# Performance work log

Measured on AMD Instinct MI355X. Metric: run time of the kernel, lower is better.

The kernel has to match this reference:

```python
import jax, jax.numpy as jnp
import numpy as np

EMBED_DIM = 768
NUM_HEADS = 12
HEAD_DIM = EMBED_DIM // NUM_HEADS
HIDDEN_DIM = int(EMBED_DIM * 4.0)
LN_EPS = 1e-5


def setup_inputs() -> dict:
    key = jax.random.key(0)
    ks = jax.random.split(key, 8)
    B, N, C = 16, 1024, EMBED_DIM
    s = 0.02
    return {
        "x": jax.random.normal(ks[0], (B, N, C), dtype=jnp.float32),
        "ln1_g": jnp.ones((C,), jnp.float32),
        "ln1_b": jnp.zeros((C,), jnp.float32),
        "qkv_w": jax.random.normal(ks[1], (C, 3 * C), jnp.float32) * s,
        "qkv_b": jnp.zeros((3 * C,), jnp.float32),
        "proj_w": jax.random.normal(ks[2], (C, C), jnp.float32) * s,
        "proj_b": jnp.zeros((C,), jnp.float32),
        "ln2_g": jnp.ones((C,), jnp.float32),
        "ln2_b": jnp.zeros((C,), jnp.float32),
        "fc1_w": jax.random.normal(ks[3], (C, HIDDEN_DIM), jnp.float32) * s,
        "fc1_b": jnp.zeros((HIDDEN_DIM,), jnp.float32),
        "fc2_w": jax.random.normal(ks[4], (HIDDEN_DIM, C), jnp.float32) * s,
        "fc2_b": jnp.zeros((C,), jnp.float32),
    }


def _layernorm(x, g, b):
    mu = jnp.mean(x, axis=-1, keepdims=True)
    var = jnp.mean(jnp.square(x - mu), axis=-1, keepdims=True)
    return (x - mu) * jax.lax.rsqrt(var + LN_EPS) * g + b


def _attention(x, qkv_w, qkv_b, proj_w, proj_b):
    B, N, C = x.shape
    qkv = x @ qkv_w + qkv_b                       # [B,N,3C]
    qkv = qkv.reshape(B, N, 3, NUM_HEADS, HEAD_DIM)
    q, k, v = qkv[:, :, 0], qkv[:, :, 1], qkv[:, :, 2]  # [B,N,H,D]
    scale = HEAD_DIM ** -0.5
    attn = jnp.einsum("bqhd,bkhd->bhqk", q, k) * scale
    attn = jax.nn.softmax(attn, axis=-1)
    out = jnp.einsum("bhqk,bkhd->bqhd", attn, v).reshape(B, N, C)
    return out @ proj_w + proj_b


def reference(x, ln1_g, ln1_b, qkv_w, qkv_b, proj_w, proj_b,
              ln2_g, ln2_b, fc1_w, fc1_b, fc2_w, fc2_b):
    x = x + _attention(_layernorm(x, ln1_g, ln1_b), qkv_w, qkv_b, proj_w, proj_b)
    h = _layernorm(x, ln2_g, ln2_b)
    h = jax.nn.gelu(h @ fc1_w + fc1_b, approximate=False)
    return x + (h @ fc2_w + fc2_b)
```

## Files before the change

### kernel.cpp

```cpp
#include <hip/hip_runtime.h>
#include <math.h>

#define SEQ 1024
#define NH 12
#define CC 768

using short8 = __attribute__((ext_vector_type(8))) short;
using bf16x8 = __attribute__((ext_vector_type(8))) __bf16;
using f32x4  = __attribute__((ext_vector_type(4))) float;

__device__ __forceinline__ unsigned short f2bf(float f){
  unsigned u = __builtin_bit_cast(unsigned, f);
  u += 0x7FFF + ((u >> 16) & 1);
  return (unsigned short)(u >> 16);
}

__device__ __forceinline__ void gload16(const void* g, void* l){
  __builtin_amdgcn_global_load_lds((const __attribute__((address_space(1))) unsigned int*)g,
                                   (__attribute__((address_space(3))) unsigned int*)l, 16, 0, 0);
}
__device__ __forceinline__ bf16x8 lds_frag(const unsigned short* p){
  return __builtin_bit_cast(bf16x8, *(const short8*)p);
}
__device__ __forceinline__ bf16x8 gld_frag(const unsigned short* p){
  return __builtin_bit_cast(bf16x8, *(const short8*)p);
}

__global__ __launch_bounds__(256) void wtrans(const float* __restrict__ W,
                                              unsigned short* __restrict__ Wt,
                                              int K, int N){
  __shared__ float tile[32][33];
  int tx = threadIdx.x & 31, ty = threadIdx.x >> 5;
  int n0 = blockIdx.x * 32, k0 = blockIdx.y * 32;
#pragma unroll
  for (int j = 0; j < 4; j++)
    tile[ty + j*8][tx] = W[(size_t)(k0 + ty + j*8) * N + n0 + tx];
  __syncthreads();
#pragma unroll
  for (int j = 0; j < 4; j++)
    Wt[(size_t)(n0 + ty + j*8) * K + k0 + tx] = f2bf(tile[tx][ty + j*8]);
}

__global__ __launch_bounds__(64) void ln_k(const float* __restrict__ x,
                                           const float* __restrict__ g,
                                           const float* __restrict__ be,
                                           unsigned short* __restrict__ out){
  const int row = blockIdx.x;
  const int lane = threadIdx.x;
  const float* xr = x + (size_t)row * CC;
  float4 v[3];
  float s = 0.f, sq = 0.f;
#pragma unroll
  for (int j = 0; j < 3; j++){
    v[j] = *(const float4*)(xr + lane*4 + j*256);
    s  += v[j].x + v[j].y + v[j].z + v[j].w;
    sq += v[j].x*v[j].x + v[j].y*v[j].y + v[j].z*v[j].z + v[j].w*v[j].w;
  }
#pragma unroll
  for (int d = 1; d < 64; d <<= 1){ s += __shfl_xor(s, d); sq += __shfl_xor(sq, d); }
  float mu = s * (1.0f/CC);
  float var = sq * (1.0f/CC) - mu*mu;
  float rstd = rsqrtf(var + 1e-5f);
  unsigned short* orow = out + (size_t)row * CC;
#pragma unroll
  for (int j = 0; j < 3; j++){
    int cb = lane*4 + j*256;
    float4 gv = *(const float4*)(g + cb);
    float4 bv = *(const float4*)(be + cb);
    ushort4 o;
    o.x = f2bf((v[j].x - mu)*rstd*gv.x + bv.x);
    o.y = f2bf((v[j].y - mu)*rstd*gv.y + bv.y);
    o.z = f2bf((v[j].z - mu)*rstd*gv.z + bv.z);
    o.w = f2bf((v[j].w - mu)*rstd*gv.w + bv.w);
    *(ushort4*)(orow + cb) = o;
  }
}

__global__ __launch_bounds__(256) void vextract(const unsigned short* __restrict__ qkv,
                                                unsigned short* __restrict__ vT){
  __shared__ unsigned short tile[32][33];
  int bh = blockIdx.y;
  int b = bh / NH, h = bh % NH;
  int tt = blockIdx.x & 31, dt = blockIdx.x >> 5;
  int tx = threadIdx.x & 31, ty = threadIdx.x >> 5;
#pragma unroll
  for (int j = 0; j < 4; j++)
    tile[ty + j*8][tx] = qkv[(size_t)(b*SEQ + tt*32 + ty + j*8)*2304 + 1536 + h*64 + dt*32 + tx];
  __syncthreads();
#pragma unroll
  for (int j = 0; j < 4; j++)
    vT[((size_t)bh*64 + dt*32 + ty + j*8)*SEQ + tt*32 + tx] = tile[tx][ty + j*8];
}

template<int MODE>
__global__ __launch_bounds__(512, 2) void gemm256(const unsigned short* __restrict__ A,
                                                  const unsigned short* __restrict__ Bt,
                                                  const float* __restrict__ bias,
                                                  const float* __restrict__ resid,
                                                  void* __restrict__ outp,
                                                  int M, int N, int K){
  __shared__ __align__(16) unsigned short lds[2][4][128*64];
  const int t = threadIdx.x;
  const int lane = t & 63, w = t >> 6;
  const int wr = w >> 2, wc = w & 3;
  const int l15 = lane & 15, lg = lane >> 4;
  const int mtiles = M >> 8;
  const int cpx = gridDim.x >> 3;
  const int bid = blockIdx.x;
  const int swz = (bid & 7) * cpx + (bid >> 3);
  const int bm = swz % mtiles, bn = swz / mtiles;

  const unsigned short* gA0 = A  + (size_t)bm*256*K;
  const unsigned short* gA1 = gA0 + (size_t)128*K;
  const unsigned short* gB0 = Bt + (size_t)bn*256*K;
  const unsigned short* gB1 = gB0 + (size_t)128*K;

  const int csw = (t & 7) ^ ((t >> 3) & 7);
  const size_t off0 = (size_t)(t >> 3)*K + csw*8;
  const size_t off1 = off0 + (size_t)64*K;

  auto stageh = [&](int bi, int rg, const unsigned short* gb, int kt){
    const unsigned short* s = gb + (size_t)kt*64;
    unsigned short* d = &lds[bi][rg][0];
    gload16(s + off0, d + t*8);
    gload16(s + off1, d + 4096 + t*8);
  };

  const int cx0 = (lg ^ (l15 & 7)) * 8;
  const int cx1 = ((4 + lg) ^ (l15 & 7)) * 8;
  const int rB = (wc & 1)*64 + l15;

  f32x4 acc[8][4] = {};
  const int nk = K >> 6;

  stageh(0,0,gA0,0); stageh(0,1,gA1,0); stageh(0,2,gB0,0); stageh(0,3,gB1,0);
  stageh(1,0,gA0,1); stageh(1,1,gA1,1); stageh(1,2,gB0,1);
  asm volatile("s_waitcnt vmcnt(6)" ::: "memory");
  __builtin_amdgcn_sched_barrier(0);
  __builtin_amdgcn_s_barrier();

  bf16x8 afr[8][2], bfl[2][2], bfh[2][2];
  for (int kt = 0; kt < nk; ++kt){
    const int buf = kt & 1;
    const unsigned short* pA = &lds[buf][wr][0];
    const unsigned short* pB = &lds[buf][2 + (wc >> 1)][0];

#pragma unroll
    for (int m = 0; m < 4; m++){
      afr[m][0] = lds_frag(pA + (m*16 + l15)*64 + cx0);
      afr[m][1] = lds_frag(pA + (m*16 + l15)*64 + cx1);
    }
#pragma unroll
    for (int n = 0; n < 2; n++){
      bfl[n][0] = lds_frag(pB + (rB + n*16)*64 + cx0);
      bfl[n][1] = lds_frag(pB + (rB + n*16)*64 + cx1);
    }
#pragma unroll
    for (int m = 4; m < 8; m++){
      afr[m][0] = lds_frag(pA + (m*16 + l15)*64 + cx0);
      afr[m][1] = lds_frag(pA + (m*16 + l15)*64 + cx1);
    }
    if (kt + 1 < nk) stageh((kt+1)&1, 3, gB1, kt+1);
    __builtin_amdgcn_sched_barrier(0);
    __builtin_amdgcn_s_barrier();
    asm volatile("s_waitcnt lgkmcnt(8)" ::: "memory");
    __builtin_amdgcn_sched_barrier(0);
    __builtin_amdgcn_s_setprio(1);
#pragma unroll
    for (int m = 0; m < 4; m++)
#pragma unroll
      for (int n = 0; n < 2; n++){
        acc[m][n] = __builtin_amdgcn_mfma_f32_16x16x32_bf16(afr[m][0], bfl[n][0], acc[m][n], 0,0,0);
        acc[m][n] = __builtin_amdgcn_mfma_f32_16x16x32_bf16(afr[m][1], bfl[n][1], acc[m][n], 0,0,0);
      }
    __builtin_amdgcn_s_setprio(0);
    __builtin_amdgcn_sched_barrier(0);
    __builtin_amdgcn_s_barrier();

#pragma unroll
    for (int n = 0; n < 2; n++){
      bfh[n][0] = lds_frag(pB + (rB + (n+2)*16)*64 + cx0);
      bfh[n][1] = lds_frag(pB + (rB + (n+2)*16)*64 + cx1);
    }
    if (kt + 2 < nk) stageh(buf, 0, gA0, kt+2);
    __builtin_amdgcn_sched_barrier(0);
    __builtin_amdgcn_s_barrier();
    asm volatile("s_waitcnt lgkmcnt(4)" ::: "memory");
    __builtin_amdgcn_sched_barrier(0);
    __builtin_amdgcn_s_setprio(1);
#pragma unroll
    for (int m = 4; m < 8; m++)
#pragma unroll
      for (int n = 0; n < 2; n++){
        acc[m][n] = __builtin_amdgcn_mfma_f32_16x16x32_bf16(afr[m][0], bfl[n][0], acc[m][n], 0,0,0);
        acc[m][n] = __builtin_amdgcn_mfma_f32_16x16x32_bf16(afr[m][1], bfl[n][1], acc[m][n], 0,0,0);
      }
    __builtin_amdgcn_s_setprio(0);
    __builtin_amdgcn_sched_barrier(0);
    __builtin_amdgcn_s_barrier();

    if (kt + 2 < nk) stageh(buf, 1, gA1, kt+2);
    __builtin_amdgcn_sched_barrier(0);
    __builtin_amdgcn_s_barrier();
    asm volatile("s_waitcnt lgkmcnt(0)" ::: "memory");
    __builtin_amdgcn_sched_barrier(0);
    __builtin_amdgcn_s_setprio(1);
#pragma unroll
    for (int m = 4; m < 8; m++)
#pragma unroll
      for (int n = 0; n < 2; n++){
        acc[m][n+2] = __builtin_amdgcn_mfma_f32_16x16x32_bf16(afr[m][0], bfh[n][0], acc[m][n+2], 0,0,0);
        acc[m][n+2] = __builtin_amdgcn_mfma_f32_16x16x32_bf16(afr[m][1], bfh[n][1], acc[m][n+2], 0,0,0);
      }
    __builtin_amdgcn_s_setprio(0);
    __builtin_amdgcn_sched_barrier(0);
    __builtin_amdgcn_s_barrier();

    if (kt + 2 < nk) stageh(buf, 2, gB0, kt+2);
    __builtin_amdgcn_sched_barrier(0);
    __builtin_amdgcn_s_barrier();
    __builtin_amdgcn_s_setprio(1);
#pragma unroll
    for (int m = 0; m < 4; m++)
#pragma unroll
      for (int n = 0; n < 2; n++){
        acc[m][n+2] = __builtin_amdgcn_mfma_f32_16x16x32_bf16(afr[m][0], bfh[n][0], acc[m][n+2], 0,0,0);
        acc[m][n+2] = __builtin_amdgcn_mfma_f32_16x16x32_bf16(afr[m][1], bfh[n][1], acc[m][n+2], 0,0,0);
      }
    __builtin_amdgcn_s_setprio(0);
    if (kt < nk - 1){
      if (kt + 2 < nk) { asm volatile("s_waitcnt vmcnt(6)" ::: "memory"); }
      else             { asm volatile("s_waitcnt vmcnt(0)" ::: "memory"); }
    }
    __builtin_amdgcn_sched_barrier(0);
    __builtin_amdgcn_s_barrier();
  }

  const int row0 = bm*256 + wr*128 + lg*4;
  const int col0 = bn*256 + wc*64 + l15;
#pragma unroll
  for (int n = 0; n < 4; n++){
    int c = col0 + n*16;
    float bv = bias[c];
#pragma unroll
    for (int m = 0; m < 8; m++){
      int r = row0 + m*16;
#pragma unroll
      for (int i = 0; i < 4; i++){
        size_t idx = (size_t)(r + i) * N + c;
        float v = acc[m][n][i] + bv;
        if constexpr (MODE == 0){
          ((unsigned short*)outp)[idx] = f2bf(v);
        } else if constexpr (MODE == 1){
          ((float*)outp)[idx] = resid[idx] + v;
        } else {
          float u = v + 0.044715f*v*v*v;
          float a = fminf(-1.5957691216057308f*u, 80.f);
          float e = __expf(a);
          float gv = 0.5f*v*(1.0f + (1.f - e)/(1.f + e));
          ((unsigned short*)outp)[idx] = f2bf(gv);
        }
      }
    }
  }
}

__global__ __launch_bounds__(256, 2) void attn_k(const unsigned short* __restrict__ qkv,
                                                 const unsigned short* __restrict__ vT,
                                                 unsigned short* __restrict__ aout){
  __shared__ __align__(16) unsigned short Ks[2][64*64];
  __shared__ __align__(16) unsigned short Vs[2][64*64];
  __shared__ __align__(16) unsigned short Ps[4][32*64];
  const int t = threadIdx.x, lane = t & 63, w = t >> 6;
  const int l15 = lane & 15, lg = lane >> 4;
  const int qt = blockIdx.x;
  const int bh = blockIdx.y;
  const int b = bh / NH, h = bh % NH;
  const size_t qrow0 = (size_t)b * SEQ + qt*128 + w*32;

  bf16x8 qf[2][2];
#pragma unroll
  for (int nf = 0; nf < 2; nf++)
#pragma unroll
    for (int ks = 0; ks < 2; ks++)
      qf[nf][ks] = gld_frag(qkv + (qrow0 + nf*16 + l15)*2304 + h*64 + ks*32 + lg*8);

  f32x4 o[2][4] = {};
  float mold[2] = {-3.0e38f, -3.0e38f};
  float lsum[2] = {0.f, 0.f};

  const unsigned short* Kgl = qkv + (size_t)b * SEQ * 2304 + 768 + h*64;
  const unsigned short* Vgl = vT + (size_t)bh * 64 * SEQ;

  auto stageKV = [&](int bufi, int kt){
#pragma unroll
    for (int i = 0; i < 2; i++){
      int idx = i*256 + t; int r = idx >> 3; int s = idx & 7; int ss = s ^ (r & 7);
      gload16(Kgl + (size_t)(kt*64 + r)*2304 + ss*8, &Ks[bufi][idx*8]);
    }
#pragma unroll
    for (int i = 0; i < 2; i++){
      int idx = i*256 + t; int r = idx >> 3; int s = idx & 7; int ss = s ^ (r & 7);
      gload16(Vgl + (size_t)r*SEQ + kt*64 + ss*8, &Vs[bufi][idx*8]);
    }
  };

  stageKV(0, 0);
  __syncthreads();
  int buf = 0;

  for (int kt = 0; kt < 16; ++kt){
    if (kt + 1 < 16) stageKV(buf ^ 1, kt + 1);

    f32x4 st[4][2] = {};
#pragma unroll
    for (int ks = 0; ks < 2; ks++){
      bf16x8 kf[4];
#pragma unroll
      for (int mf = 0; mf < 4; mf++){
        int rr = mf*16 + l15;
        int sc = (ks*4 + lg) ^ (rr & 7);
        kf[mf] = lds_frag(&Ks[buf][rr*64 + sc*8]);
      }
#pragma unroll
      for (int mf = 0; mf < 4; mf++)
#pragma unroll
        for (int nf = 0; nf < 2; nf++)
          st[mf][nf] = __builtin_amdgcn_mfma_f32_16x16x32_bf16(kf[mf], qf[nf][ks], st[mf][nf], 0, 0, 0);
    }

    float fsc[2];
#pragma unroll
    for (int nf = 0; nf < 2; nf++){
      float mx = -3.0e38f;
#pragma unroll
      for (int mf = 0; mf < 4; mf++)
#pragma unroll
        for (int i = 0; i < 4; i++){
          float sv = st[mf][nf][i] * 0.125f;
          st[mf][nf][i] = sv;
          mx = fmaxf(mx, sv);
        }
      mx = fmaxf(mx, __shfl_xor(mx, 16));
      mx = fmaxf(mx, __shfl_xor(mx, 32));
      float nm = fmaxf(mold[nf], mx);
      float f = __expf(mold[nf] - nm);
      mold[nf] = nm;
      float rs = 0.f;
#pragma unroll
      for (int mf = 0; mf < 4; mf++)
#pragma unroll
        for (int i = 0; i < 4; i++){
          float p = __expf(st[mf][nf][i] - nm);
          st[mf][nf][i] = p;
          rs += p;
        }
      rs += __shfl_xor(rs, 16);
      rs += __shfl_xor(rs, 32);
      lsum[nf] = lsum[nf]*f + rs;
      fsc[nf] = f;
    }

#pragma unroll
    for (int nf = 0; nf < 2; nf++)
#pragma unroll
      for (int mf = 0; mf < 4; mf++)
#pragma unroll
        for (int i = 0; i < 4; i++){
          int rP = nf*16 + l15;
          int col = mf*16 + lg*4 + i;
          Ps[w][rP*64 + (col ^ ((rP & 7) << 3))] = f2bf(st[mf][nf][i]);
        }

#pragma unroll
    for (int mm = 0; mm < 2; mm++)
#pragma unroll
      for (int i = 0; i < 4; i++){
        float fo = __shfl(fsc[mm], lg*4 + i);
#pragma unroll
        for (int df = 0; df < 4; df++)
          o[mm][df][i] *= fo;
      }

#pragma unroll
    for (int ks = 0; ks < 2; ks++){
      bf16x8 pf[2], vf[4];
#pragma unroll
      for (int mm = 0; mm < 2; mm++){
        int rP = mm*16 + l15;
        int sc = (ks*4 + lg) ^ (rP & 7);
        pf[mm] = lds_frag(&Ps[w][rP*64 + sc*8]);
      }
#pragma unroll
      for (int df = 0; df < 4; df++){
        int rr = df*16 + l15;
        int sc = (ks*4 + lg) ^ (rr & 7);
        vf[df] = lds_frag(&Vs[buf][rr*64 + sc*8]);
      }
#pragma unroll
      for (int mm = 0; mm < 2; mm++)
#pragma unroll
        for (int df = 0; df < 4; df++)
          o[mm][df] = __builtin_amdgcn_mfma_f32_16x16x32_bf16(pf[mm], vf[df], o[mm][df], 0, 0, 0);
    }
    __syncthreads();
    buf ^= 1;
  }

#pragma unroll
  for (int mm = 0; mm < 2; mm++){
    float li = 1.0f / lsum[mm];
#pragma unroll
    for (int i = 0; i < 4; i++){
      float rl = __shfl(li, lg*4 + i);
      size_t r = qrow0 + mm*16 + lg*4 + i;
#pragma unroll
      for (int df = 0; df < 4; df++)
        aout[r*CC + h*64 + df*16 + l15] = f2bf(o[mm][df][i] * rl);
    }
  }
}

extern "C" void kernel_launch(void* const* d_in, const int* in_sizes, int n_in,
                              void* d_out, int out_size, void* d_ws, size_t ws_size,
                              hipStream_t stream){
  (void)in_sizes; (void)n_in; (void)out_size; (void)ws_size;
  const float* x      = (const float*)d_in[0];
  const float* ln1_g  = (const float*)d_in[1];
  const float* ln1_b  = (const float*)d_in[2];
  const float* qkv_w  = (const float*)d_in[3];
  const float* qkv_b  = (const float*)d_in[4];
  const float* proj_w = (const float*)d_in[5];
  const float* proj_b = (const float*)d_in[6];
  const float* ln2_g  = (const float*)d_in[7];
  const float* ln2_b  = (const float*)d_in[8];
  const float* fc1_w  = (const float*)d_in[9];
  const float* fc1_b  = (const float*)d_in[10];
  const float* fc2_w  = (const float*)d_in[11];
  const float* fc2_b  = (const float*)d_in[12];
  float* out = (float*)d_out;
  char* ws = (char*)d_ws;

  unsigned short* ln_out  = (unsigned short*)(ws);
  unsigned short* qkv_buf = (unsigned short*)(ws + 25165824);
  unsigned short* vTb     = (unsigned short*)(ws + 100663296);
  unsigned short* attn    = (unsigned short*)(ws + 125829120);
  unsigned short* hbuf    = qkv_buf;
  char* wbase = ws + 150994944;
  unsigned short* wq = (unsigned short*)(wbase);
  unsigned short* wp = (unsigned short*)(wbase + 3538944);
  unsigned short* w1 = (unsigned short*)(wbase + 4718592);
  unsigned short* w2 = (unsigned short*)(wbase + 9437184);

  wtrans<<<dim3(72, 24), 256, 0, stream>>>(qkv_w, wq, 768, 2304);
  wtrans<<<dim3(24, 24), 256, 0, stream>>>(proj_w, wp, 768, 768);
  wtrans<<<dim3(96, 24), 256, 0, stream>>>(fc1_w, w1, 768, 3072);
  wtrans<<<dim3(24, 96), 256, 0, stream>>>(fc2_w, w2, 3072, 768);

  ln_k<<<16384, 64, 0, stream>>>(x, ln1_g, ln1_b, ln_out);
  gemm256<0><<<64*9, 512, 0, stream>>>(ln_out, wq, qkv_b, nullptr, qkv_buf, 16384, 2304, 768);
  vextract<<<dim3(64, 192), 256, 0, stream>>>(qkv_buf, vTb);
  attn_k<<<dim3(8, 192), 256, 0, stream>>>(qkv_buf, vTb, attn);
  gemm256<1><<<64*3, 512, 0, stream>>>(attn, wp, proj_b, x, out, 16384, 768, 768);
  ln_k<<<16384, 64, 0, stream>>>(out, ln2_g, ln2_b, ln_out);
  gemm256<2><<<64*12, 512, 0, stream>>>(ln_out, w1, fc1_b, nullptr, hbuf, 16384, 3072, 768);
  gemm256<1><<<64*3, 512, 0, stream>>>(hbuf, w2, fc2_b, out, out, 16384, 768, 3072);
}
```

Measured before the change: 635.1 us.

## Split A fragments into halves, drop block swizzle, pack bf16 epilogue stores

Result: slower. 662.0 us (+4.2%).

```diff
diff --git a/kernel.cpp b/kernel.cpp
--- a/kernel.cpp
+++ b/kernel.cpp
@@ -104,11 +104,9 @@
   const int lane = t & 63, w = t >> 6;
   const int wr = w >> 2, wc = w & 3;
   const int l15 = lane & 15, lg = lane >> 4;
-  const int mtiles = M >> 8;
-  const int cpx = gridDim.x >> 3;
+  const int ntn = N >> 8;
   const int bid = blockIdx.x;
-  const int swz = (bid & 7) * cpx + (bid >> 3);
-  const int bm = swz % mtiles, bn = swz / mtiles;
+  const int bm = bid / ntn, bn = bid % ntn;
 
   const unsigned short* gA0 = A  + (size_t)bm*256*K;
   const unsigned short* gA1 = gA0 + (size_t)128*K;
@@ -139,7 +137,7 @@
   __builtin_amdgcn_sched_barrier(0);
   __builtin_amdgcn_s_barrier();
 
-  bf16x8 afr[8][2], bfl[2][2], bfh[2][2];
+  bf16x8 alo[4][2], ahi[4][2], bfl[2][2], bfh[2][2];
   for (int kt = 0; kt < nk; ++kt){
     const int buf = kt & 1;
     const unsigned short* pA = &lds[buf][wr][0];
@@ -147,31 +145,48 @@
 
 #pragma unroll
     for (int m = 0; m < 4; m++){
-      afr[m][0] = lds_frag(pA + (m*16 + l15)*64 + cx0);
-      afr[m][1] = lds_frag(pA + (m*16 + l15)*64 + cx1);
+      alo[m][0] = lds_frag(pA + (m*16 + l15)*64 + cx0);
+      alo[m][1] = lds_frag(pA + (m*16 + l15)*64 + cx1);
     }
 #pragma unroll
     for (int n = 0; n < 2; n++){
       bfl[n][0] = lds_frag(pB + (rB + n*16)*64 + cx0);
       bfl[n][1] = lds_frag(pB + (rB + n*16)*64 + cx1);
     }
-#pragma unroll
-    for (int m = 4; m < 8; m++){
-      afr[m][0] = lds_frag(pA + (m*16 + l15)*64 + cx0);
-      afr[m][1] = lds_frag(pA + (m*16 + l15)*64 + cx1);
-    }
     if (kt + 1 < nk) stageh((kt+1)&1, 3, gB1, kt+1);
     __builtin_amdgcn_sched_barrier(0);
     __builtin_amdgcn_s_barrier();
-    asm volatile("s_waitcnt lgkmcnt(8)" ::: "memory");
+    asm volatile("s_waitcnt lgkmcnt(0)" ::: "memory");
     __builtin_amdgcn_sched_barrier(0);
     __builtin_amdgcn_s_setprio(1);
 #pragma unroll
     for (int m = 0; m < 4; m++)
 #pragma unroll
       for (int n = 0; n < 2; n++){
-        acc[m][n] = __builtin_amdgcn_mfma_f32_16x16x32_bf16(afr[m][0], bfl[n][0], acc[m][n], 0,0,0);
-        acc[m][n] = __builtin_amdgcn_mfma_f32_16x16x32_bf16(afr[m][1], bfl[n][1], acc[m][n], 0,0,0);
+        acc[m][n] = __builtin_amdgcn_mfma_f32_16x16x32_bf16(alo[m][0], bfl[n][0], acc[m][n], 0,0,0);
+        acc[m][n] = __builtin_amdgcn_mfma_f32_16x16x32_bf16(alo[m][1], bfl[n][1], acc[m][n], 0,0,0);
+      }
+    __builtin_amdgcn_s_setprio(0);
+    __builtin_amdgcn_sched_barrier(0);
+    __builtin_amdgcn_s_barrier();
+
+#pragma unroll
+    for (int m = 0; m < 4; m++){
+      ahi[m][0] = lds_frag(pA + ((m+4)*16 + l15)*64 + cx0);
+      ahi[m][1] = lds_frag(pA + ((m+4)*16 + l15)*64 + cx1);
+    }
+    if (kt + 2 < nk) stageh(buf, 0, gA0, kt+2);
+    __builtin_amdgcn_sched_barrier(0);
+    __builtin_amdgcn_s_barrier();
+    asm volatile("s_waitcnt lgkmcnt(0)" ::: "memory");
+    __builtin_amdgcn_sched_barrier(0);
+    __builtin_amdgcn_s_setprio(1);
+#pragma unroll
+    for (int m = 0; m < 4; m++)
+#pragma unroll
+      for (int n = 0; n < 2; n++){
+        acc[m+4][n] = __builtin_amdgcn_mfma_f32_16x16x32_bf16(ahi[m][0], bfl[n][0], acc[m+4][n], 0,0,0);
+        acc[m+4][n] = __builtin_amdgcn_mfma_f32_16x16x32_bf16(ahi[m][1], bfl[n][1], acc[m+4][n], 0,0,0);
       }
     __builtin_amdgcn_s_setprio(0);
     __builtin_amdgcn_sched_barrier(0);
@@ -182,50 +197,33 @@
       bfh[n][0] = lds_frag(pB + (rB + (n+2)*16)*64 + cx0);
       bfh[n][1] = lds_frag(pB + (rB + (n+2)*16)*64 + cx1);
     }
-    if (kt + 2 < nk) stageh(buf, 0, gA0, kt+2);
-    __builtin_amdgcn_sched_barrier(0);
-    __builtin_amdgcn_s_barrier();
-    asm volatile("s_waitcnt lgkmcnt(4)" ::: "memory");
+    if (kt + 2 < nk) stageh(buf, 1, gA1, kt+2);
+    __builtin_amdgcn_sched_barrier(0);
+    __builtin_amdgcn_s_barrier();
+    asm volatile("s_waitcnt lgkmcnt(0)" ::: "memory");
     __builtin_amdgcn_sched_barrier(0);
     __builtin_amdgcn_s_setprio(1);
 #pragma unroll
-    for (int m = 4; m < 8; m++)
+    for (int m = 0; m < 4; m++)
 #pragma unroll
       for (int n = 0; n < 2; n++){
-        acc[m][n] = __builtin_amdgcn_mfma_f32_16x16x32_bf16(afr[m][0], bfl[n][0], acc[m][n], 0,0,0);
-        acc[m][n] = __builtin_amdgcn_mfma_f32_16x16x32_bf16(afr[m][1], bfl[n][1], acc[m][n], 0,0,0);
+        acc[m+4][n+2] = __builtin_amdgcn_mfma_f32_16x16x32_bf16(ahi[m][0], bfh[n][0], acc[m+4][n+2], 0,0,0);
+        acc[m+4][n+2] = __builtin_amdgcn_mfma_f32_16x16x32_bf16(ahi[m][1], bfh[n][1], acc[m+4][n+2], 0,0,0);
       }
     __builtin_amdgcn_s_setprio(0);
     __builtin_amdgcn_sched_barrier(0);
     __builtin_amdgcn_s_barrier();
 
-    if (kt + 2 < nk) stageh(buf, 1, gA1, kt+2);
-    __builtin_amdgcn_sched_barrier(0);
-    __builtin_amdgcn_s_barrier();
-    asm volatile("s_waitcnt lgkmcnt(0)" ::: "memory");
-    __builtin_amdgcn_sched_barrier(0);
+    if (kt + 2 < nk) stageh(buf, 2, gB0, kt+2);
+    __builtin_amdgcn_sched_barrier(0);
+    __builtin_amdgcn_s_barrier();
     __builtin_amdgcn_s_setprio(1);
 #pragma unroll
-    for (int m = 4; m < 8; m++)
+    for (int m = 0; m < 4; m++)
 #pragma unroll
       for (int n = 0; n < 2; n++){
-        acc[m][n+2] = __builtin_amdgcn_mfma_f32_16x16x32_bf16(afr[m][0], bfh[n][0], acc[m][n+2], 0,0,0);
-        acc[m][n+2] = __builtin_amdgcn_mfma_f32_16x16x32_bf16(afr[m][1], bfh[n][1], acc[m][n+2], 0,0,0);
-      }
-    __builtin_amdgcn_s_setprio(0);
-    __builtin_amdgcn_sched_barrier(0);
-    __builtin_amdgcn_s_barrier();
-
-    if (kt + 2 < nk) stageh(buf, 2, gB0, kt+2);
-    __builtin_amdgcn_sched_barrier(0);
-    __builtin_amdgcn_s_barrier();
-    __builtin_amdgcn_s_setprio(1);
-#pragma unroll
-    for (int m = 0; m < 4; m++)
-#pragma unroll
-      for (int n = 0; n < 2; n++){
-        acc[m][n+2] = __builtin_amdgcn_mfma_f32_16x16x32_bf16(afr[m][0], bfh[n][0], acc[m][n+2], 0,0,0);
-        acc[m][n+2] = __builtin_amdgcn_mfma_f32_16x16x32_bf16(afr[m][1], bfh[n][1], acc[m][n+2], 0,0,0);
+        acc[m][n+2] = __builtin_amdgcn_mfma_f32_16x16x32_bf16(alo[m][0], bfh[n][0], acc[m][n+2], 0,0,0);
+        acc[m][n+2] = __builtin_amdgcn_mfma_f32_16x16x32_bf16(alo[m][1], bfh[n][1], acc[m][n+2], 0,0,0);
       }
     __builtin_amdgcn_s_setprio(0);
     if (kt < nk - 1){
@@ -237,31 +235,61 @@
   }
 
   const int row0 = bm*256 + wr*128 + lg*4;
-  const int col0 = bn*256 + wc*64 + l15;
-#pragma unroll
-  for (int n = 0; n < 4; n++){
-    int c = col0 + n*16;
-    float bv = bias[c];
-#pragma unroll
-    for (int m = 0; m < 8; m++){
-      int r = row0 + m*16;
-#pragma unroll
-      for (int i = 0; i < 4; i++){
-        size_t idx = (size_t)(r + i) * N + c;
-        float v = acc[m][n][i] + bv;
-        if constexpr (MODE == 0){
-          ((unsigned short*)outp)[idx] = f2bf(v);
-        } else if constexpr (MODE == 1){
-          ((float*)outp)[idx] = resid[idx] + v;
-        } else {
-          float u = v + 0.044715f*v*v*v;
-          float a = fminf(-1.5957691216057308f*u, 80.f);
-          float e = __expf(a);
-          float gv = 0.5f*v*(1.0f + (1.f - e)/(1.f + e));
-          ((unsigned short*)outp)[idx] = f2bf(gv);
-        }
-      }
-    }
+  const int col0 = bn*256 + wc*64;
+  if constexpr (MODE == 1){
+#pragma unroll
+    for (int n = 0; n < 4; n++){
+      int c = col0 + n*16 + l15;
+      float bv = bias[c];
+#pragma unroll
+      for (int m = 0; m < 8; m++){
+        int r = row0 + m*16;
+#pragma unroll
+        for (int i = 0; i < 4; i++){
+          size_t idx = (size_t)(r + i) * N + c;
+          ((float*)outp)[idx] = resid[idx] + acc[m][n][i] + bv;
+        }
+      }
+    }
+  } else {
+#pragma unroll
+    for (int n = 0; n < 4; n++){
+      float bv = bias[col0 + n*16 + l15];
+#pragma unroll
+      for (int m = 0; m < 8; m++)
+#pragma unroll
+        for (int i = 0; i < 4; i++){
+          float v = acc[m][n][i] + bv;
+          if constexpr (MODE == 2){
+            float u = v + 0.044715f*v*v*v;
+            float a = fminf(-1.5957691216057308f*u, 80.f);
+            float e = __expf(a);
+            v = 0.5f*v*(1.0f + (1.f - e)/(1.f + e));
+          }
+          acc[m][n][i] = v;
+        }
+    }
+    unsigned int* O = (unsigned int*)outp;
+    const int src0 = lg*16 + ((2*l15) & 15);
+    const int src1 = lg*16 + ((2*l15 + 1) & 15);
+    const bool sel = (l15 < 8);
+#pragma unroll
+    for (int p = 0; p < 2; p++)
+#pragma unroll
+      for (int m = 0; m < 8; m++)
+#pragma unroll
+        for (int i = 0; i < 4; i++){
+          float e0a = __shfl(acc[m][2*p][i],   src0);
+          float e0b = __shfl(acc[m][2*p+1][i], src0);
+          float e1a = __shfl(acc[m][2*p][i],   src1);
+          float e1b = __shfl(acc[m][2*p+1][i], src1);
+          float v0 = sel ? e0a : e0b;
+          float v1 = sel ? e1a : e1b;
+          unsigned int pk = (unsigned int)f2bf(v0) | ((unsigned int)f2bf(v1) << 16);
+          int r = row0 + m*16 + i;
+          int cu = (col0 + p*32)/2 + l15;
+          O[(size_t)r * (N >> 1) + cu] = pk;
+        }
   }
 }
 
```
